# Optimization experiments

Hardware: AMD Instinct MI355X
Metric: run time of the kernel (lower is better)

Reference implementation:

```python
import jax, jax.numpy as jnp
import numpy as np

B, L, D, V = 2048, 32, 256, 100000  # batch, sentence length, embed dim, vocab
KW = 3  # kernel_width (forced to 3 by the module's shape arithmetic)


def conv_h(x, w, b):
    """1-channel conv over the seq axis, kernel (3,1), pad 2 -> length L+2. x:(B,L,D), w:(3,)."""
    xp = jnp.pad(x, ((0, 0), (2, 2), (0, 0)))
    L_out = x.shape[1] + 2
    out = w[0] * xp[:, 0:L_out] + w[1] * xp[:, 1:L_out + 1] + w[2] * xp[:, 2:L_out + 2]
    return out + b


def avgpool3(x):
    """avg_pool2d kernel (3,1) stride 1 along seq axis. (B,L+2,D) -> (B,L,D)."""
    return (x[:, :-2] + x[:, 1:-1] + x[:, 2:]) / 3.0


def conv3d_21(x, w, b):
    """Conv3d kernel (2,3,1), pad (0,2,0). x:(B,2,L,D), w:(2,3) -> (B,L+2,D)."""
    xp = jnp.pad(x, ((0, 0), (0, 0), (2, 2), (0, 0)))
    L_out = x.shape[2] + 2
    out = jnp.zeros((x.shape[0], L_out, x.shape[3]), dtype=x.dtype)
    for d0 in range(2):
        for k in range(3):
            out = out + w[d0, k] * xp[:, d0, k:k + L_out]
    return out + b


def euclid_attention(a, b):
    """A[k,i,j] = 1/(1 + ||a[k,i]-b[k,j]||_2), computed via the matmul cdist trick."""
    a2 = jnp.sum(a * a, axis=-1)  # (B,La)
    b2 = jnp.sum(b * b, axis=-1)  # (B,Lb)
    d2 = a2[:, :, None] + b2[:, None, :] - 2.0 * jnp.einsum('bid,bjd->bij', a, b)
    d = jnp.sqrt(jnp.maximum(d2, 0.0))
    return 1.0 / (1.0 + d)


def setup_inputs() -> dict:
    key = jax.random.key(0)
    ks = jax.random.split(key, 16)
    inp = {
        'sentence1': jax.random.randint(ks[0], (B, L), 0, V),
        'sentence2': jax.random.randint(ks[1], (B, L), 0, V),
        'embed': jax.random.normal(ks[2], (V, D), dtype=jnp.float32) * 0.05,
        'c1w': jax.random.normal(ks[3], (KW,), dtype=jnp.float32) * 0.3,
        'c1b': jax.random.normal(ks[4], (), dtype=jnp.float32) * 0.05,
        'c2w': jax.random.normal(ks[5], (KW,), dtype=jnp.float32) * 0.3,
        'c2b': jax.random.normal(ks[6], (), dtype=jnp.float32) * 0.05,
        'c3w': jax.random.normal(ks[7], (2, KW), dtype=jnp.float32) * 0.3,
        'c3b': jax.random.normal(ks[8], (), dtype=jnp.float32) * 0.05,
        'W0': jax.random.normal(ks[9], (L, D), dtype=jnp.float32),
        'W1': jax.random.normal(ks[10], (L, D), dtype=jnp.float32),
        'fw1': jax.random.normal(ks[11], (2 * D, 64), dtype=jnp.float32) * 0.05,
        'fb1': jnp.zeros((64,), dtype=jnp.float32),
        'fw2': jax.random.normal(ks[12], (64, 2), dtype=jnp.float32) * 0.1,
        'fb2': jnp.zeros((2,), dtype=jnp.float32),
    }
    return inp


def reference(sentence1, sentence2, embed, c1w, c1b, c2w, c2b, c3w, c3b, W0, W1, fw1, fb1, fw2, fb2):
    e1 = embed[sentence1]                      # (B,L,D)
    e2 = embed[sentence2]
    rep1 = avgpool3(conv_h(e1, c1w, c1b))      # (B,L,D)
    rep2 = avgpool3(conv_h(e2, c1w, c1b))
    A1 = euclid_attention(rep1, rep2)          # (B,L,L)
    att1 = jnp.einsum('bij,jd->bid', A1, W0)   # (B,L,D)
    att2 = jnp.einsum('bij,jd->bid', A1, W1)
    c1 = conv3d_21(jnp.stack([rep1, att1], axis=1), c3w, c3b)  # (B,L+2,D)
    c2 = conv3d_21(jnp.stack([rep2, att2], axis=1), c3w, c3b)
    A2 = euclid_attention(c1, c2)              # (B,L+2,L+2)
    col = jnp.sum(A2, axis=2)                  # (B,L+2)
    row = jnp.sum(A2, axis=1)
    ca1 = avgpool3(c1 * col[:, :, None])       # (B,L,D)
    ca2 = avgpool3(c2 * row[:, :, None])
    v1 = jnp.mean(conv_h(ca1, c2w, c2b), axis=1)  # (B,D)
    v2 = jnp.mean(conv_h(ca2, c2w, c2b), axis=1)
    h = jnp.tanh(jnp.concatenate([v1, v2], axis=1) @ fw1 + fb1)
    logits = h @ fw2 + fb2                     # (B,2)
    return jax.nn.softmax(logits, axis=0)      # faithful: original Softmax(dim=0)
```

## Files before the change

### kernel.cpp

```cpp
#include <hip/hip_runtime.h>
#include <math.h>

#define NB 2048
#define LL 32
#define DD 256
#define LP 34
#define SRH 264
#define SA 35
#define BMS 40

typedef unsigned short u16;
typedef short bf8 __attribute__((ext_vector_type(8)));
typedef float f32x4 __attribute__((ext_vector_type(4)));

__device__ __forceinline__ float bf_lo(unsigned u) { return __uint_as_float(u << 16); }
__device__ __forceinline__ float bf_hi(unsigned u) { return __uint_as_float(u & 0xffff0000u); }
__device__ __forceinline__ float bfu(u16 h) { return __uint_as_float(((unsigned)h) << 16); }
__device__ __forceinline__ u16 f2bf(float f) {
    unsigned u = __float_as_uint(f);
    u += 0x7fffu + ((u >> 16) & 1u);
    return (u16)(u >> 16);
}

__global__ __launch_bounds__(256)
void pack_w(const float* __restrict__ W0, const float* __restrict__ W1, u16* __restrict__ wp)
{
    const int t = blockIdx.x * 256 + threadIdx.x;
    const int lane = t & 63, nt = (t >> 6) & 15, wsel = t >> 10;
    const float* W = wsel ? W1 : W0;
    const int col = nt * 16 + (lane & 15);
    const int k0 = (lane >> 4) * 8;
    unsigned d[4];
    #pragma unroll
    for (int q = 0; q < 4; ++q) {
        const u16 lo = f2bf(W[(size_t)(k0 + 2 * q) * DD + col]);
        const u16 hi = f2bf(W[(size_t)(k0 + 2 * q + 1) * DD + col]);
        d[q] = (unsigned)lo | ((unsigned)hi << 16);
    }
    uint4 u; u.x = d[0]; u.y = d[1]; u.z = d[2]; u.w = d[3];
    ((uint4*)wp)[t] = u;
}

__global__ __launch_bounds__(256, 3)
void abcnn_fused(const int* __restrict__ s1, const int* __restrict__ s2,
                 const float* __restrict__ embed,
                 const float* __restrict__ c1w, const float* __restrict__ c1b,
                 const float* __restrict__ c2w, const float* __restrict__ c2b,
                 const float* __restrict__ c3w, const float* __restrict__ c3b,
                 const float* __restrict__ W0, const float* __restrict__ W1,
                 const float* __restrict__ fw1, const float* __restrict__ fb1,
                 const float* __restrict__ fw2, const float* __restrict__ fb2,
                 const u16* __restrict__ wpack, float* __restrict__ lgts)
{
    __shared__ __align__(16) u16 RC[2][LP][SRH];
    __shared__ float AU[LP * SA];
    __shared__ __align__(16) u16 Bm[LP][BMS];
    __shared__ float nrm[2][LP];
    __shared__ float UN[900];

    const int b    = blockIdx.x;
    const int tid  = threadIdx.x;
    const int lane = tid & 63;
    const int wv   = tid >> 6;

    {
        const float w0 = c1w[0], w1 = c1w[1], w2 = c1w[2], bb = c1b[0];
        const float gm2 = w0 * (1.f/3.f);
        const float gm1 = (w0 + w1) * (1.f/3.f);
        const float g0  = (w0 + w1 + w2) * (1.f/3.f);
        const float gp1 = (w1 + w2) * (1.f/3.f);
        const float gp2 = w2 * (1.f/3.f);
        for (int s = 0; s < 2; ++s) {
            const int* sent = (s == 0 ? s1 : s2) + b * LL;
            float rep[LL];
            #pragma unroll
            for (int j = 0; j < LL; ++j) rep[j] = bb;
            #pragma unroll
            for (int jj = 0; jj < LL; ++jj) {
                const float x = embed[(size_t)sent[jj] * DD + tid];
                if (jj >= 2)      rep[jj - 2] += gp2 * x;
                if (jj >= 1)      rep[jj - 1] += gp1 * x;
                                  rep[jj    ] += g0  * x;
                if (jj <= LL - 2) rep[jj + 1] += gm1 * x;
                if (jj <= LL - 3) rep[jj + 2] += gm2 * x;
            }
            #pragma unroll
            for (int j = 0; j < LL; ++j) RC[s][j][tid] = f2bf(rep[j]);
        }
    }
    __syncthreads();

    f32x4 g2acc = {0.f, 0.f, 0.f, 0.f};
    {
        if (tid < 64) {
            const int s = tid >> 5, r = tid & 31;
            const uint4* rp = (const uint4*)&RC[s][r][0];
            float acc = 0.f;
            #pragma unroll 8
            for (int q = 0; q < 32; ++q) {
                const uint4 u = rp[q];
                float a;
                a = bf_lo(u.x); acc += a * a;  a = bf_hi(u.x); acc += a * a;
                a = bf_lo(u.y); acc += a * a;  a = bf_hi(u.y); acc += a * a;
                a = bf_lo(u.z); acc += a * a;  a = bf_hi(u.z); acc += a * a;
                a = bf_lo(u.w); acc += a * a;  a = bf_hi(u.w); acc += a * a;
            }
            nrm[s][r] = acc;
        }
        const int mt = wv >> 1, nt = wv & 1;
        const int ar = mt * 16 + (lane & 15);
        const int br = nt * 16 + (lane & 15);
        const int ko = (lane >> 4) * 8;
        #pragma unroll
        for (int ks = 0; ks < 8; ++ks) {
            const bf8 a = *(const bf8*)&RC[0][ar][ks * 32 + ko];
            const bf8 bb2 = *(const bf8*)&RC[1][br][ks * 32 + ko];
            g2acc = __builtin_amdgcn_mfma_f32_16x16x32_bf16(a, bb2, g2acc, 0, 0, 0);
        }
    }
    __syncthreads();
    {
        const int mt = wv >> 1, nt = wv & 1;
        #pragma unroll
        for (int r = 0; r < 4; ++r) {
            const int i = mt * 16 + (lane >> 4) * 4 + r;
            const int j = nt * 16 + (lane & 15);
            const float d2 = nrm[0][i] + nrm[1][j] - 2.f * g2acc[r];
            AU[i * SA + j] = 1.f / (1.f + sqrtf(fmaxf(d2, 0.f)));
        }
    }
    __syncthreads();

    {
        const float cw10 = c3w[3], cw11 = c3w[4], cw12 = c3w[5];
        for (int e = tid; e < LP * 32; e += 256) {
            const int i = e >> 5, m = e & 31;
            float acc = 0.f;
            if (i >= 2)           acc += cw10 * AU[(i - 2) * SA + m];
            if (i >= 1 && i < 33) acc += cw11 * AU[(i - 1) * SA + m];
            if (i < 32)           acc += cw12 * AU[i * SA + m];
            Bm[i][m] = f2bf(acc);
        }
    }
    __syncthreads();

    {
        const float cw00 = c3w[0], cw01 = c3w[1], cw02 = c3w[2], cb3 = c3b[0];
        for (int wsel = 0; wsel < 2; ++wsel) {
            const float* W = wsel ? W1 : W0;
            bf8 bfr[4];
            #pragma unroll
            for (int n = 0; n < 4; ++n)
                bfr[n] = *(const bf8*)(wpack + ((size_t)((wsel * 16 + (wv * 4 + n)) * 64 + lane)) * 8);
            bf8 afr[2];
            #pragma unroll
            for (int mt = 0; mt < 2; ++mt)
                afr[mt] = *(const bf8*)&Bm[mt * 16 + (lane & 15)][(lane >> 4) * 8];
            f32x4 dacc[2][4];
            #pragma unroll
            for (int mt = 0; mt < 2; ++mt)
                #pragma unroll
                for (int n = 0; n < 4; ++n) {
                    const f32x4 z = {0.f, 0.f, 0.f, 0.f};
                    dacc[mt][n] = __builtin_amdgcn_mfma_f32_16x16x32_bf16(afr[mt], bfr[n], z, 0, 0, 0);
                }
            #pragma unroll
            for (int mt = 0; mt < 2; ++mt) {
                const int i0 = mt * 16 + (lane >> 4) * 4;
                #pragma unroll
                for (int n = 0; n < 4; ++n) {
                    const int d = (wv * 4 + n) * 16 + (lane & 15);
                    float t[6];
                    #pragma unroll
                    for (int q = 0; q < 6; ++q) {
                        const int rr = i0 - 2 + q;
                        t[q] = (rr >= 0 && rr < LL) ? bfu(RC[wsel][rr][d]) : 0.f;
                    }
                    #pragma unroll
                    for (int r = 0; r < 4; ++r)
                        dacc[mt][n][r] += cb3 + cw00 * t[r] + cw01 * t[r + 1] + cw02 * t[r + 2];
                }
            }
            float s32 = cb3 + cw00 * bfu(RC[wsel][30][tid]) + cw01 * bfu(RC[wsel][31][tid]);
            float s33 = cb3 + cw00 * bfu(RC[wsel][31][tid]);
            #pragma unroll
            for (int m = 0; m < 32; ++m) {
                const float wvv = W[(size_t)m * DD + tid];
                s32 += bfu(Bm[32][m]) * wvv;
                s33 += bfu(Bm[33][m]) * wvv;
            }
            __syncthreads();
            #pragma unroll
            for (int mt = 0; mt < 2; ++mt)
                #pragma unroll
                for (int n = 0; n < 4; ++n)
                    #pragma unroll
                    for (int r = 0; r < 4; ++r) {
                        const int i = mt * 16 + (lane >> 4) * 4 + r;
                        const int d = (wv * 4 + n) * 16 + (lane & 15);
                        RC[wsel][i][d] = f2bf(dacc[mt][n][r]);
                    }
            RC[wsel][32][tid] = f2bf(s32);
            RC[wsel][33][tid] = f2bf(s33);
            __syncthreads();
        }
    }

    {
        if (tid < 68) {
            const int s = (tid < 34) ? 0 : 1;
            const int r = (tid < 34) ? tid : tid - 34;
            const uint4* rp = (const uint4*)&RC[s][r][0];
            float acc = 0.f;
            #pragma unroll 8
            for (int q = 0; q < 32; ++q) {
                const uint4 u = rp[q];
                float a;
                a = bf_lo(u.x); acc += a * a;  a = bf_hi(u.x); acc += a * a;
                a = bf_lo(u.y); acc += a * a;  a = bf_hi(u.y); acc += a * a;
                a = bf_lo(u.z); acc += a * a;  a = bf_hi(u.z); acc += a * a;
                a = bf_lo(u.w); acc += a * a;  a = bf_hi(u.w); acc += a * a;
            }
            nrm[s][r] = acc;
        }
        g2acc[0] = 0.f; g2acc[1] = 0.f; g2acc[2] = 0.f; g2acc[3] = 0.f;
        const int mt = wv >> 1, nt = wv & 1;
        const int ar = mt * 16 + (lane & 15);
        const int br = nt * 16 + (lane & 15);
        const int ko = (lane >> 4) * 8;
        #pragma unroll
        for (int ks = 0; ks < 8; ++ks) {
            const bf8 a = *(const bf8*)&RC[0][ar][ks * 32 + ko];
            const bf8 bb2 = *(const bf8*)&RC[1][br][ks * 32 + ko];
            g2acc = __builtin_amdgcn_mfma_f32_16x16x32_bf16(a, bb2, g2acc, 0, 0, 0);
        }
    }
    __syncthreads();
    {
        const int mt = wv >> 1, nt = wv & 1;
        #pragma unroll
        for (int r = 0; r < 4; ++r) {
            const int i = mt * 16 + (lane >> 4) * 4 + r;
            const int j = nt * 16 + (lane & 15);
            const float d2 = nrm[0][i] + nrm[1][j] - 2.f * g2acc[r];
            AU[i * SA + j] = 1.f / (1.f + sqrtf(fmaxf(d2, 0.f)));
        }
        if (tid < 132) {
            int i, j;
            if (tid < 34)       { i = 32;        j = tid; }
            else if (tid < 68)  { i = 33;        j = tid - 34; }
            else if (tid < 100) { i = tid - 68;  j = 32; }
            else                { i = tid - 100; j = 33; }
            const uint4* ap = (const uint4*)&RC[0][i][0];
            const uint4* bp = (const uint4*)&RC[1][j][0];
            float g = 0.f;
            #pragma unroll 4
            for (int q = 0; q < 32; ++q) {
                const uint4 ua = ap[q], ub = bp[q];
                g += bf_lo(ua.x) * bf_lo(ub.x) + bf_hi(ua.x) * bf_hi(ub.x);
                g += bf_lo(ua.y) * bf_lo(ub.y) + bf_hi(ua.y) * bf_hi(ub.y);
                g += bf_lo(ua.z) * bf_lo(ub.z) + bf_hi(ua.z) * bf_hi(ub.z);
                g += bf_lo(ua.w) * bf_lo(ub.w) + bf_hi(ua.w) * bf_hi(ub.w);
            }
            const float d2 = nrm[0][i] + nrm[1][j] - 2.f * g;
            AU[i * SA + j] = 1.f / (1.f + sqrtf(fmaxf(d2, 0.f)));
        }
    }
    __syncthreads();

    {
        const float S2 = c2w[0] + c2w[1] + c2w[2];
        const float sc = S2 * (1.f / 102.f);
        if (tid < 68) {
            const bool isCol = tid < 34;
            const int p = isCol ? tid : tid - 34;
            float s = 0.f;
            for (int q = 0; q < LP; ++q) s += AU[isCol ? (p * SA + q) : (q * SA + p)];
            const float cnt = (p == 0 || p == 33) ? 1.f : ((p == 1 || p == 32) ? 2.f : 3.f);
            UN[tid] = s * cnt * sc;
        }
    }
    __syncthreads();

    {
        const float cb2 = c2b[0];
        float v1 = cb2, v2 = cb2;
        #pragma unroll
        for (int p = 0; p < LP; ++p) {
            v1 += UN[p]      * bfu(RC[0][p][tid]);
            v2 += UN[34 + p] * bfu(RC[1][p][tid]);
        }
        UN[68 + tid]       = v1;
        UN[68 + 256 + tid] = v2;
    }
    __syncthreads();

    {
        const int u = tid & 63, sg = tid >> 6;
        const float* vv = &UN[68];
        const float* fp = fw1 + (size_t)(sg * 128) * 64 + u;
        float part = 0.f;
        for (int t = 0; t < 128; ++t) part += vv[sg * 128 + t] * fp[(size_t)t * 64];
        UN[580 + tid] = part;
    }
    __syncthreads();
    if (tid < 64) {
        const float hsum = UN[580 + tid] + UN[644 + tid] + UN[708 + tid] + UN[772 + tid] + fb1[tid];
        UN[836 + tid] = tanhf(hsum);
    }
    __syncthreads();
    if (tid < 2) {
        float lg = fb2[tid];
        for (int u2 = 0; u2 < 64; ++u2) lg += UN[836 + u2] * fw2[u2 * 2 + tid];
        lgts[tid * NB + b] = lg;
    }
}

__global__ __launch_bounds__(1024)
void softmax_dim0(const float* __restrict__ lgts, float* __restrict__ out)
{
    __shared__ float red[17];
    const int tid = threadIdx.x;
    for (int c = 0; c < 2; ++c) {
        const float x0 = lgts[c * NB + tid];
        const float x1 = lgts[c * NB + 1024 + tid];
        float m = fmaxf(x0, x1);
        #pragma unroll
        for (int off = 32; off >= 1; off >>= 1) m = fmaxf(m, __shfl_xor(m, off));
        if ((tid & 63) == 0) red[tid >> 6] = m;
        __syncthreads();
        if (tid == 0) { float t = red[0]; for (int i = 1; i < 16; ++i) t = fmaxf(t, red[i]); red[16] = t; }
        __syncthreads();
        m = red[16];
        const float e0 = expf(x0 - m), e1 = expf(x1 - m);
        float s = e0 + e1;
        #pragma unroll
        for (int off = 32; off >= 1; off >>= 1) s += __shfl_xor(s, off);
        if ((tid & 63) == 0) red[tid >> 6] = s;
        __syncthreads();
        if (tid == 0) { float t = 0.f; for (int i = 0; i < 16; ++i) t += red[i]; red[16] = t; }
        __syncthreads();
        const float inv = 1.f / red[16];
        out[(size_t)tid * 2 + c]          = e0 * inv;
        out[(size_t)(1024 + tid) * 2 + c] = e1 * inv;
        __syncthreads();
    }
}

extern "C" void kernel_launch(void* const* d_in, const int* in_sizes, int n_in,
                              void* d_out, int out_size, void* d_ws, size_t ws_size,
                              hipStream_t stream)
{
    (void)in_sizes; (void)n_in; (void)out_size; (void)ws_size;
    const int*   s1  = (const int*)  d_in[0];
    const int*   s2  = (const int*)  d_in[1];
    const float* emb = (const float*)d_in[2];
    const float* c1w = (const float*)d_in[3];
    const float* c1b = (const float*)d_in[4];
    const float* c2w = (const float*)d_in[5];
    const float* c2b = (const float*)d_in[6];
    const float* c3w = (const float*)d_in[7];
    const float* c3b = (const float*)d_in[8];
    const float* W0  = (const float*)d_in[9];
    const float* W1  = (const float*)d_in[10];
    const float* fw1 = (const float*)d_in[11];
    const float* fb1 = (const float*)d_in[12];
    const float* fw2 = (const float*)d_in[13];
    const float* fb2 = (const float*)d_in[14];
    u16*   wpack = (u16*)d_ws;
    float* lgts  = (float*)((char*)d_ws + 32768);
    float* out   = (float*)d_out;

    pack_w<<<dim3(8), dim3(256), 0, stream>>>(W0, W1, wpack);
    abcnn_fused<<<dim3(NB), dim3(256), 0, stream>>>(s1, s2, emb, c1w, c1b, c2w, c2b,
                                                    c3w, c3b, W0, W1, fw1, fb1, fw2, fb2,
                                                    wpack, lgts);
    softmax_dim0<<<dim3(1), dim3(1024), 0, stream>>>(lgts, out);
}
```

Measured before the change: 83.05 us.

## Compute norms and edge rows via MFMA tiles, split embedding gather across sentences

The embedding gather now has each half of the block handle one sentence with float2 loads, instead of looping over both sentences with scalar loads. Row norms come from the diagonal of MFMA Gram tiles (self-products) rather than scalar loops. The 34-row second-stage matmuls use overlapping 16-row tiles at offset 18, replacing the scalar fallback code for rows 32-33. Packed bf16 conversion uses v_cvt_pk_bf16_f32. This moves scalar work onto matrix cores at the cost of some redundant MFMA tiles and extra barriers.

```diff
diff --git a/kernel.cpp b/kernel.cpp
--- a/kernel.cpp
+++ b/kernel.cpp
@@ -12,15 +12,42 @@
 typedef unsigned short u16;
 typedef short bf8 __attribute__((ext_vector_type(8)));
 typedef float f32x4 __attribute__((ext_vector_type(4)));
-
+typedef float vf2 __attribute__((ext_vector_type(2)));
+
+__device__ __forceinline__ float bfu(u16 h) { return __uint_as_float(((unsigned)h) << 16); }
 __device__ __forceinline__ float bf_lo(unsigned u) { return __uint_as_float(u << 16); }
 __device__ __forceinline__ float bf_hi(unsigned u) { return __uint_as_float(u & 0xffff0000u); }
-__device__ __forceinline__ float bfu(u16 h) { return __uint_as_float(((unsigned)h) << 16); }
 __device__ __forceinline__ u16 f2bf(float f) {
     unsigned u = __float_as_uint(f);
     u += 0x7fffu + ((u >> 16) & 1u);
     return (u16)(u >> 16);
 }
+__device__ __forceinline__ unsigned cvt_pk_bf(float lo, float hi) {
+    unsigned r;
+    asm("v_cvt_pk_bf16_f32 %0, %1, %2" : "=v"(r) : "v"(lo), "v"(hi));
+    return r;
+}
+
+__device__ __forceinline__ f32x4 gram8(const u16* __restrict__ A, const u16* __restrict__ B) {
+    f32x4 acc = {0.f, 0.f, 0.f, 0.f};
+    #pragma unroll
+    for (int ks = 0; ks < 8; ++ks) {
+        const bf8 a = *(const bf8*)(A + ks * 32);
+        const bf8 b = *(const bf8*)(B + ks * 32);
+        acc = __builtin_amdgcn_mfma_f32_16x16x32_bf16(a, b, acc, 0, 0, 0);
+    }
+    return acc;
+}
+
+__device__ static const signed char TB2[8][4] = {
+    {0,0,1,0}, {0,0,1,16}, {0,16,1,0}, {0,16,1,16},
+    {0,0,0,0}, {0,16,0,16}, {1,0,1,0}, {1,16,1,16}};
+
+__device__ static const signed char TB5[15][4] = {
+    {0,0,0,0}, {0,16,0,16}, {0,18,0,18}, {1,0,1,0}, {1,16,1,16}, {1,18,1,18},
+    {0,0,1,0},  {0,0,1,16},  {0,0,1,18},
+    {0,16,1,0}, {0,16,1,16}, {0,16,1,18},
+    {0,18,1,0}, {0,18,1,16}, {0,18,1,18}};
 
 __global__ __launch_bounds__(256)
 void pack_w(const float* __restrict__ W0, const float* __restrict__ W1, u16* __restrict__ wp)
@@ -47,7 +74,6 @@
                  const float* __restrict__ c1w, const float* __restrict__ c1b,
                  const float* __restrict__ c2w, const float* __restrict__ c2b,
                  const float* __restrict__ c3w, const float* __restrict__ c3b,
-                 const float* __restrict__ W0, const float* __restrict__ W1,
                  const float* __restrict__ fw1, const float* __restrict__ fb1,
                  const float* __restrict__ fw2, const float* __restrict__ fb2,
                  const u16* __restrict__ wpack, float* __restrict__ lgts)
@@ -62,6 +88,9 @@
     const int tid  = threadIdx.x;
     const int lane = tid & 63;
     const int wv   = tid >> 6;
+    const int c15  = lane & 15;
+    const int q4x  = (lane >> 4) * 4;
+    const int ko   = (lane >> 4) * 8;
 
     {
         const float w0 = c1w[0], w1 = c1w[1], w2 = c1w[2], bb = c1b[0];
@@ -70,63 +99,56 @@
         const float g0  = (w0 + w1 + w2) * (1.f/3.f);
         const float gp1 = (w1 + w2) * (1.f/3.f);
         const float gp2 = w2 * (1.f/3.f);
-        for (int s = 0; s < 2; ++s) {
-            const int* sent = (s == 0 ? s1 : s2) + b * LL;
-            float rep[LL];
-            #pragma unroll
-            for (int j = 0; j < LL; ++j) rep[j] = bb;
-            #pragma unroll
-            for (int jj = 0; jj < LL; ++jj) {
-                const float x = embed[(size_t)sent[jj] * DD + tid];
-                if (jj >= 2)      rep[jj - 2] += gp2 * x;
-                if (jj >= 1)      rep[jj - 1] += gp1 * x;
-                                  rep[jj    ] += g0  * x;
-                if (jj <= LL - 2) rep[jj + 1] += gm1 * x;
-                if (jj <= LL - 3) rep[jj + 2] += gm2 * x;
-            }
-            #pragma unroll
-            for (int j = 0; j < LL; ++j) RC[s][j][tid] = f2bf(rep[j]);
-        }
-    }
-    __syncthreads();
-
-    f32x4 g2acc = {0.f, 0.f, 0.f, 0.f};
-    {
-        if (tid < 64) {
-            const int s = tid >> 5, r = tid & 31;
-            const uint4* rp = (const uint4*)&RC[s][r][0];
-            float acc = 0.f;
-            #pragma unroll 8
-            for (int q = 0; q < 32; ++q) {
-                const uint4 u = rp[q];
-                float a;
-                a = bf_lo(u.x); acc += a * a;  a = bf_hi(u.x); acc += a * a;
-                a = bf_lo(u.y); acc += a * a;  a = bf_hi(u.y); acc += a * a;
-                a = bf_lo(u.z); acc += a * a;  a = bf_hi(u.z); acc += a * a;
-                a = bf_lo(u.w); acc += a * a;  a = bf_hi(u.w); acc += a * a;
-            }
-            nrm[s][r] = acc;
-        }
-        const int mt = wv >> 1, nt = wv & 1;
-        const int ar = mt * 16 + (lane & 15);
-        const int br = nt * 16 + (lane & 15);
-        const int ko = (lane >> 4) * 8;
-        #pragma unroll
-        for (int ks = 0; ks < 8; ++ks) {
-            const bf8 a = *(const bf8*)&RC[0][ar][ks * 32 + ko];
-            const bf8 bb2 = *(const bf8*)&RC[1][br][ks * 32 + ko];
-            g2acc = __builtin_amdgcn_mfma_f32_16x16x32_bf16(a, bb2, g2acc, 0, 0, 0);
-        }
-    }
-    __syncthreads();
-    {
-        const int mt = wv >> 1, nt = wv & 1;
-        #pragma unroll
-        for (int r = 0; r < 4; ++r) {
-            const int i = mt * 16 + (lane >> 4) * 4 + r;
-            const int j = nt * 16 + (lane & 15);
-            const float d2 = nrm[0][i] + nrm[1][j] - 2.f * g2acc[r];
-            AU[i * SA + j] = 1.f / (1.f + sqrtf(fmaxf(d2, 0.f)));
+        const int s  = tid >> 7;
+        const int dp = tid & 127;
+        const int* sent = (s ? s2 : s1) + b * LL;
+        vf2 rep[LL];
+        #pragma unroll
+        for (int j = 0; j < LL; ++j) rep[j] = (vf2){bb, bb};
+        #pragma unroll
+        for (int jj = 0; jj < LL; ++jj) {
+            const int idx = sent[jj];
+            const vf2 x = *(const vf2*)(embed + (size_t)idx * DD + 2 * dp);
+            if (jj >= 2)      rep[jj - 2] += gp2 * x;
+            if (jj >= 1)      rep[jj - 1] += gp1 * x;
+                              rep[jj    ] += g0  * x;
+            if (jj <= LL - 2) rep[jj + 1] += gm1 * x;
+            if (jj <= LL - 3) rep[jj + 2] += gm2 * x;
+        }
+        #pragma unroll
+        for (int j = 0; j < LL; ++j)
+            *(unsigned*)&RC[s][j][2 * dp] = cvt_pk_bf(rep[j].x, rep[j].y);
+    }
+    __syncthreads();
+
+    {
+        f32x4 h2[2];
+        #pragma unroll
+        for (int k = 0; k < 2; ++k) {
+            const int t  = wv * 2 + k;
+            const int sa = TB2[t][0], oa = TB2[t][1], sb = TB2[t][2], ob = TB2[t][3];
+            const f32x4 G = gram8(&RC[sa][oa + c15][ko], &RC[sb][ob + c15][ko]);
+            h2[k] = G;
+            if (t >= 4 && (c15 >> 2) == (lane >> 4)) {
+                const int r = c15 & 3;
+                const float dv = (r == 0) ? G[0] : (r == 1) ? G[1] : (r == 2) ? G[2] : G[3];
+                nrm[sa][oa + c15] = dv;
+            }
+        }
+        __syncthreads();
+        #pragma unroll
+        for (int k = 0; k < 2; ++k) {
+            const int t = wv * 2 + k;
+            if (t < 4) {
+                const int oa = TB2[t][1], ob = TB2[t][3];
+                const f32x4 G = h2[k];
+                #pragma unroll
+                for (int r = 0; r < 4; ++r) {
+                    const int i = oa + q4x + r, j = ob + c15;
+                    const float d2 = nrm[0][i] + nrm[1][j] - 2.f * G[r];
+                    AU[i * SA + j] = 1.f / (1.f + sqrtf(fmaxf(d2, 0.f)));
+                }
+            }
         }
     }
     __syncthreads();
@@ -147,123 +169,79 @@
     {
         const float cw00 = c3w[0], cw01 = c3w[1], cw02 = c3w[2], cb3 = c3b[0];
         for (int wsel = 0; wsel < 2; ++wsel) {
-            const float* W = wsel ? W1 : W0;
-            bf8 bfr[4];
+            f32x4 acc[12];
             #pragma unroll
-            for (int n = 0; n < 4; ++n)
-                bfr[n] = *(const bf8*)(wpack + ((size_t)((wsel * 16 + (wv * 4 + n)) * 64 + lane)) * 8);
-            bf8 afr[2];
-            #pragma unroll
-            for (int mt = 0; mt < 2; ++mt)
-                afr[mt] = *(const bf8*)&Bm[mt * 16 + (lane & 15)][(lane >> 4) * 8];
-            f32x4 dacc[2][4];
-            #pragma unroll
-            for (int mt = 0; mt < 2; ++mt)
+            for (int k = 0; k < 12; ++k) {
+                const int t  = wv + 4 * k;
+                const int rq = t >> 4;
+                const int ro = (rq == 0) ? 0 : (rq == 1) ? 16 : 18;
+                const int n  = t & 15;
+                const bf8 a = *(const bf8*)&Bm[ro + c15][ko];
+                const bf8 w = *(const bf8*)(wpack + (size_t)((wsel * 16 + n) * 64 + lane) * 8);
+                const f32x4 z = {0.f, 0.f, 0.f, 0.f};
+                acc[k] = __builtin_amdgcn_mfma_f32_16x16x32_bf16(a, w, z, 0, 0, 0);
+                const int d  = n * 16 + c15;
+                const int i0 = ro + q4x;
+                float tt[6];
                 #pragma unroll
-                for (int n = 0; n < 4; ++n) {
-                    const f32x4 z = {0.f, 0.f, 0.f, 0.f};
-                    dacc[mt][n] = __builtin_amdgcn_mfma_f32_16x16x32_bf16(afr[mt], bfr[n], z, 0, 0, 0);
+                for (int q2 = 0; q2 < 6; ++q2) {
+                    const int rr = i0 - 2 + q2;
+                    tt[q2] = (rr >= 0 && rr < LL) ? bfu(RC[wsel][rr][d]) : 0.f;
                 }
-            #pragma unroll
-            for (int mt = 0; mt < 2; ++mt) {
-                const int i0 = mt * 16 + (lane >> 4) * 4;
                 #pragma unroll
-                for (int n = 0; n < 4; ++n) {
-                    const int d = (wv * 4 + n) * 16 + (lane & 15);
-                    float t[6];
-                    #pragma unroll
-                    for (int q = 0; q < 6; ++q) {
-                        const int rr = i0 - 2 + q;
-                        t[q] = (rr >= 0 && rr < LL) ? bfu(RC[wsel][rr][d]) : 0.f;
-                    }
-                    #pragma unroll
-                    for (int r = 0; r < 4; ++r)
-                        dacc[mt][n][r] += cb3 + cw00 * t[r] + cw01 * t[r + 1] + cw02 * t[r + 2];
-                }
-            }
-            float s32 = cb3 + cw00 * bfu(RC[wsel][30][tid]) + cw01 * bfu(RC[wsel][31][tid]);
-            float s33 = cb3 + cw00 * bfu(RC[wsel][31][tid]);
-            #pragma unroll
-            for (int m = 0; m < 32; ++m) {
-                const float wvv = W[(size_t)m * DD + tid];
-                s32 += bfu(Bm[32][m]) * wvv;
-                s33 += bfu(Bm[33][m]) * wvv;
+                for (int r = 0; r < 4; ++r)
+                    acc[k][r] += cb3 + cw00 * tt[r] + cw01 * tt[r + 1] + cw02 * tt[r + 2];
             }
             __syncthreads();
             #pragma unroll
-            for (int mt = 0; mt < 2; ++mt)
+            for (int k = 0; k < 12; ++k) {
+                const int t  = wv + 4 * k;
+                const int rq = t >> 4;
+                const int ro = (rq == 0) ? 0 : (rq == 1) ? 16 : 18;
+                const int n  = t & 15;
+                const int d  = n * 16 + c15;
+                const int i0 = ro + q4x;
+                const unsigned p01 = cvt_pk_bf(acc[k][0], acc[k][1]);
+                const unsigned p23 = cvt_pk_bf(acc[k][2], acc[k][3]);
+                RC[wsel][i0    ][d] = (u16)p01;
+                RC[wsel][i0 + 1][d] = (u16)(p01 >> 16);
+                RC[wsel][i0 + 2][d] = (u16)p23;
+                RC[wsel][i0 + 3][d] = (u16)(p23 >> 16);
+            }
+            __syncthreads();
+        }
+    }
+
+    {
+        f32x4 h5[4];
+        #pragma unroll
+        for (int k = 0; k < 4; ++k) {
+            const int t = wv + 4 * k;
+            if (t < 15) {
+                const int sa = TB5[t][0], oa = TB5[t][1], sb = TB5[t][2], ob = TB5[t][3];
+                const f32x4 G = gram8(&RC[sa][oa + c15][ko], &RC[sb][ob + c15][ko]);
+                h5[k] = G;
+                if (t < 6 && (c15 >> 2) == (lane >> 4)) {
+                    const int r = c15 & 3;
+                    const float dv = (r == 0) ? G[0] : (r == 1) ? G[1] : (r == 2) ? G[2] : G[3];
+                    nrm[sa][oa + c15] = dv;
+                }
+            }
+        }
+        __syncthreads();
+        #pragma unroll
+        for (int k = 0; k < 4; ++k) {
+            const int t = wv + 4 * k;
+            if (t >= 6 && t < 15) {
+                const int oa = TB5[t][1], ob = TB5[t][3];
+                const f32x4 G = h5[k];
                 #pragma unroll
-                for (int n = 0; n < 4; ++n)
-                    #pragma unroll
-                    for (int r = 0; r < 4; ++r) {
-                        const int i = mt * 16 + (lane >> 4) * 4 + r;
-                        const int d = (wv * 4 + n) * 16 + (lane & 15);
-                        RC[wsel][i][d] = f2bf(dacc[mt][n][r]);
-                    }
-            RC[wsel][32][tid] = f2bf(s32);
-            RC[wsel][33][tid] = f2bf(s33);
-            __syncthreads();
-        }
-    }
-
-    {
-        if (tid < 68) {
-            const int s = (tid < 34) ? 0 : 1;
-            const int r = (tid < 34) ? tid : tid - 34;
-            const uint4* rp = (const uint4*)&RC[s][r][0];
-            float acc = 0.f;
-            #pragma unroll 8
-            for (int q = 0; q < 32; ++q) {
-                const uint4 u = rp[q];
-                float a;
-                a = bf_lo(u.x); acc += a * a;  a = bf_hi(u.x); acc += a * a;
-                a = bf_lo(u.y); acc += a * a;  a = bf_hi(u.y); acc += a * a;
-                a = bf_lo(u.z); acc += a * a;  a = bf_hi(u.z); acc += a * a;
-                a = bf_lo(u.w); acc += a * a;  a = bf_hi(u.w); acc += a * a;
-            }
-            nrm[s][r] = acc;
-        }
-        g2acc[0] = 0.f; g2acc[1] = 0.f; g2acc[2] = 0.f; g2acc[3] = 0.f;
-        const int mt = wv >> 1, nt = wv & 1;
-        const int ar = mt * 16 + (lane & 15);
-        const int br = nt * 16 + (lane & 15);
-        const int ko = (lane >> 4) * 8;
-        #pragma unroll
-        for (int ks = 0; ks < 8; ++ks) {
-            const bf8 a = *(const bf8*)&RC[0][ar][ks * 32 + ko];
-            const bf8 bb2 = *(const bf8*)&RC[1][br][ks * 32 + ko];
-            g2acc = __builtin_amdgcn_mfma_f32_16x16x32_bf16(a, bb2, g2acc, 0, 0, 0);
-        }
-    }
-    __syncthreads();
-    {
-        const int mt = wv >> 1, nt = wv & 1;
-        #pragma unroll
-        for (int r = 0; r < 4; ++r) {
-            const int i = mt * 16 + (lane >> 4) * 4 + r;
-            const int j = nt * 16 + (lane & 15);
-            const float d2 = nrm[0][i] + nrm[1][j] - 2.f * g2acc[r];
-            AU[i * SA + j] = 1.f / (1.f + sqrtf(fmaxf(d2, 0.f)));
-        }
-        if (tid < 132) {
-            int i, j;
-            if (tid < 34)       { i = 32;        j = tid; }
-            else if (tid < 68)  { i = 33;        j = tid - 34; }
-            else if (tid < 100) { i = tid - 68;  j = 32; }
-            else                { i = tid - 100; j = 33; }
-            const uint4* ap = (const uint4*)&RC[0][i][0];
-            const uint4* bp = (const uint4*)&RC[1][j][0];
-            float g = 0.f;
-            #pragma unroll 4
-            for (int q = 0; q < 32; ++q) {
-                const uint4 ua = ap[q], ub = bp[q];
-                g += bf_lo(ua.x) * bf_lo(ub.x) + bf_hi(ua.x) * bf_hi(ub.x);
-                g += bf_lo(ua.y) * bf_lo(ub.y) + bf_hi(ua.y) * bf_hi(ub.y);
-                g += bf_lo(ua.z) * bf_lo(ub.z) + bf_hi(ua.z) * bf_hi(ub.z);
-                g += bf_lo(ua.w) * bf_lo(ub.w) + bf_hi(ua.w) * bf_hi(ub.w);
-            }
-            const float d2 = nrm[0][i] + nrm[1][j] - 2.f * g;
-            AU[i * SA + j] = 1.f / (1.f + sqrtf(fmaxf(d2, 0.f)));
+                for (int r = 0; r < 4; ++r) {
+                    const int i = oa + q4x + r, j = ob + c15;
+                    const float d2 = nrm[0][i] + nrm[1][j] - 2.f * G[r];
+                    AU[i * SA + j] = 1.f / (1.f + sqrtf(fmaxf(d2, 0.f)));
+                }
+            }
         }
     }
     __syncthreads();
@@ -373,7 +351,7 @@
 
     pack_w<<<dim3(8), dim3(256), 0, stream>>>(W0, W1, wpack);
     abcnn_fused<<<dim3(NB), dim3(256), 0, stream>>>(s1, s2, emb, c1w, c1b, c2w, c2b,
-                                                    c3w, c3b, W0, W1, fw1, fb1, fw2, fb2,
+                                                    c3w, c3b, fw1, fb1, fw2, fb2,
                                                     wpack, lgts);
     softmax_dim0<<<dim3(1), dim3(1024), 0, stream>>>(lgts, out);
 }
```

After: 81.63 us. Within noise of the previous version (-1.7%).
